# Kernel tuning notes

Measured on AMD Instinct MI355X. Metric: run time of the kernel, lower is better.

The kernel has to match this reference:

```python
import jax, jax.numpy as jnp
import numpy as np
from jax import lax

B, T, N, FI, FO, K = 32, 128, 200, 32, 64, 3
STRIDE, PAD, DIL = 1, 1, 1


def setup_inputs() -> dict:
    key = jax.random.key(0)
    k1, k2, k3 = jax.random.split(key, 3)
    bound = 1.0 / np.sqrt(FI * K)
    x = jax.random.normal(k1, (B, T, N, FI), dtype=jnp.float32)
    weight = jax.random.uniform(k2, (N * FO, FI, K), dtype=jnp.float32,
                                minval=-bound, maxval=bound)
    bias = jax.random.uniform(k3, (N, FO), dtype=jnp.float32,
                              minval=-bound, maxval=bound)
    return {"x": x, "weight": weight, "bias": bias}


def reference(x, weight, bias):
    # x: [B, T, N, FI] -> [B, N*FI, T]   (rearrange '... t n f -> ... (n f) t')
    b, t, n, fi = x.shape
    fo = bias.shape[1]
    xc = jnp.transpose(x, (0, 2, 3, 1)).reshape(b, n * fi, t)
    # Grouped conv1d: one group per instance (n groups), weight [N*FO, FI, K]
    out = lax.conv_general_dilated(
        xc, weight,
        window_strides=(STRIDE,),
        padding=[(PAD, PAD)],
        rhs_dilation=(DIL,),
        feature_group_count=n,
        dimension_numbers=("NCH", "OIH", "NCH"),
    )  # [B, N*FO, T_out]
    t_out = out.shape[-1]
    # rearrange '... (n f) t -> ... t n f'
    out = jnp.transpose(out.reshape(b, n, fo, t_out), (0, 3, 1, 2))
    return out + bias  # bias broadcasts over [B, T_out, N, FO]
```

## Files before the change

kernel.cpp:

```cpp
#include <hip/hip_runtime.h>
#include <hip/hip_bf16.h>
#include <cstddef>

#define B_ 32
#define T_ 128
#define N_ 200
#define FI_ 32
#define FO_ 64
#define K_ 3

typedef __attribute__((ext_vector_type(8))) short short8;
typedef __attribute__((ext_vector_type(8))) unsigned short ushort8;
typedef __attribute__((ext_vector_type(4))) float f32x4;

#define AROW_ 40
#define A_ROWS_ (T_ + 2)
#define B_OFF_ (A_ROWS_ * AROW_)
#define BROW_ 40
#define BK_SZ_ (FO_ * BROW_)

__device__ __forceinline__ unsigned short f2bf(float f) {
    union { __hip_bfloat16 h; unsigned short u; } cv;
    cv.h = __float2bfloat16(f);
    return cv.u;
}

__global__ void conv_prep(const float* __restrict__ w,
                          unsigned short* __restrict__ wbf) {
    const int idx = blockIdx.x * 256 + threadIdx.x;
    if (idx >= N_ * FO_) return;
    const float* wp = w + (size_t)idx * (FI_ * K_);
    float v[FI_ * K_];
    #pragma unroll
    for (int j = 0; j < (FI_ * K_) / 4; ++j) {
        const float4 t4 = *reinterpret_cast<const float4*>(&wp[j * 4]);
        v[j*4+0] = t4.x; v[j*4+1] = t4.y; v[j*4+2] = t4.z; v[j*4+3] = t4.w;
    }
    const int n = idx >> 6, f = idx & 63;
    #pragma unroll
    for (int tap = 0; tap < K_; ++tap) {
        ushort8 u[4];
        #pragma unroll
        for (int i = 0; i < FI_; ++i) u[i >> 3][i & 7] = f2bf(v[i * K_ + tap]);
        unsigned short* dst = wbf + (((size_t)n * K_ + tap) * FO_ + f) * FI_;
        #pragma unroll
        for (int q = 0; q < 4; ++q)
            *reinterpret_cast<ushort8*>(&dst[q * 8]) = u[q];
    }
}

template <bool PREW>
__global__ __launch_bounds__(256, 6) void conv_main(
    const float* __restrict__ x, const float* __restrict__ w,
    const unsigned short* __restrict__ wbf,
    const float* __restrict__ bias, float* __restrict__ out)
{
    __shared__ __align__(16) unsigned short lds[B_OFF_ + K_ * BK_SZ_];

    const int bid = blockIdx.x;
    const int b = bid & 31;
    const int n = bid >> 5;
    const int tid = threadIdx.x;
    const int lane = tid & 63;
    const int wv = tid >> 6;

    if constexpr (PREW) {
        const unsigned short* src = wbf + (size_t)n * K_ * FO_ * FI_;
        #pragma unroll
        for (int ss = 0; ss < 3; ++ss) {
            const int s = tid + ss * 256;
            const int tf = s >> 2;
            const int q = s & 3;
            const ushort8 u = *reinterpret_cast<const ushort8*>(&src[tf * FI_ + q * 8]);
            *reinterpret_cast<ushort8*>(
                &lds[B_OFF_ + (tf >> 6) * BK_SZ_ + (tf & 63) * BROW_ + q * 8]) = u;
        }
    } else {
        const int f = tid >> 2;
        const int i0 = (tid & 3) * 8;
        const float* wp = w + ((size_t)n * FO_ + f) * (FI_ * K_) + (size_t)i0 * K_;
        float v[24];
        #pragma unroll
        for (int j = 0; j < 6; ++j) {
            const float4 t4 = *reinterpret_cast<const float4*>(&wp[j * 4]);
            v[j*4+0] = t4.x; v[j*4+1] = t4.y; v[j*4+2] = t4.z; v[j*4+3] = t4.w;
        }
        #pragma unroll
        for (int k = 0; k < K_; ++k) {
            ushort8 u;
            #pragma unroll
            for (int j = 0; j < 8; ++j) u[j] = f2bf(v[j * K_ + k]);
            *reinterpret_cast<ushort8*>(&lds[B_OFF_ + k * BK_SZ_ + f * BROW_ + i0]) = u;
        }
    }

    const float* xb = x + ((size_t)b * T_ * N_ + n) * FI_;
    for (int s = tid; s < A_ROWS_ * 4; s += 256) {
        const int rr = s >> 2, q = s & 3;
        const int t = rr - 1;
        ushort8 u = (ushort8)0;
        if (t >= 0 && t < T_) {
            const float4 v0 = *reinterpret_cast<const float4*>(
                &xb[(size_t)t * N_ * FI_ + q * 8]);
            const float4 v1 = *reinterpret_cast<const float4*>(
                &xb[(size_t)t * N_ * FI_ + q * 8 + 4]);
            u[0] = f2bf(v0.x); u[1] = f2bf(v0.y); u[2] = f2bf(v0.z); u[3] = f2bf(v0.w);
            u[4] = f2bf(v1.x); u[5] = f2bf(v1.y); u[6] = f2bf(v1.z); u[7] = f2bf(v1.w);
        }
        *reinterpret_cast<ushort8*>(&lds[rr * AROW_ + q * 8]) = u;
    }

    __syncthreads();

    f32x4 acc[2][4];
    #pragma unroll
    for (int m = 0; m < 2; ++m)
        #pragma unroll
        for (int j = 0; j < 4; ++j)
            acc[m][j] = (f32x4){0.f, 0.f, 0.f, 0.f};

    const int row16 = lane & 15;
    const int grp = lane >> 4;

    #pragma unroll
    for (int k = 0; k < K_; ++k) {
        const short8 a0 = *reinterpret_cast<const short8*>(
            &lds[(wv * 32 + 0  + row16 + k) * AROW_ + grp * 8]);
        const short8 a1 = *reinterpret_cast<const short8*>(
            &lds[(wv * 32 + 16 + row16 + k) * AROW_ + grp * 8]);
        #pragma unroll
        for (int j = 0; j < 4; ++j) {
            const short8 bf = *reinterpret_cast<const short8*>(
                &lds[B_OFF_ + k * BK_SZ_ + (j * 16 + row16) * BROW_ + grp * 8]);
            acc[0][j] = __builtin_amdgcn_mfma_f32_16x16x32_bf16(a0, bf, acc[0][j], 0, 0, 0);
            acc[1][j] = __builtin_amdgcn_mfma_f32_16x16x32_bf16(a1, bf, acc[1][j], 0, 0, 0);
        }
    }

    #pragma unroll
    for (int j = 0; j < 4; ++j) {
        const float bv = bias[n * FO_ + j * 16 + row16];
        #pragma unroll
        for (int m = 0; m < 2; ++m) {
            #pragma unroll
            for (int r = 0; r < 4; ++r) {
                const int t = wv * 32 + m * 16 + grp * 4 + r;
                out[(((size_t)b * T_ + t) * N_ + n) * FO_ + j * 16 + row16] =
                    acc[m][j][r] + bv;
            }
        }
    }
}

extern "C" void kernel_launch(void* const* d_in, const int* in_sizes, int n_in,
                              void* d_out, int out_size, void* d_ws, size_t ws_size,
                              hipStream_t stream) {
    const float* x    = (const float*)d_in[0];
    const float* w    = (const float*)d_in[1];
    const float* bias = (const float*)d_in[2];
    float* out = (float*)d_out;

    const size_t W_BF_BYTES = (size_t)N_ * K_ * FO_ * FI_ * 2;
    const int grid = B_ * N_;

    if (ws_size >= W_BF_BYTES) {
        unsigned short* wbf = (unsigned short*)d_ws;
        conv_prep<<<(N_ * FO_ + 255) / 256, 256, 0, stream>>>(w, wbf);
        conv_main<true><<<grid, 256, 0, stream>>>(x, w, wbf, bias, out);
    } else {
        conv_main<false><<<grid, 256, 0, stream>>>(x, w, nullptr, bias, out);
    }
}
```

Baseline: 94.70 us.

## Load weight MFMA fragments directly from global memory instead of staging in LDS

The main kernel no longer copies the per-instance bf16 weight tile into shared memory. Each wave now reads its B-operand fragments straight from the prepacked global buffer, which L2 serves since all 32 batch blocks of an instance share the same weights. This shrinks LDS use from about 35 KB to about 10 KB per block, which could raise occupancy, and removes the LDS write/read round-trip. The prep kernel is also spread over four times more threads, each converting one 8-element chunk. The cost is redundant global and L2 traffic, since every wave reloads the weights, and MFMA issue may stall on global-memory latency.

```diff
diff --git a/kernel.cpp b/kernel.cpp
--- a/kernel.cpp
+++ b/kernel.cpp
@@ -15,9 +15,6 @@
 
 #define AROW_ 40
 #define A_ROWS_ (T_ + 2)
-#define B_OFF_ (A_ROWS_ * AROW_)
-#define BROW_ 40
-#define BK_SZ_ (FO_ * BROW_)
 
 __device__ __forceinline__ unsigned short f2bf(float f) {
     union { __hip_bfloat16 h; unsigned short u; } cv;
@@ -28,24 +25,25 @@
 __global__ void conv_prep(const float* __restrict__ w,
                           unsigned short* __restrict__ wbf) {
     const int idx = blockIdx.x * 256 + threadIdx.x;
-    if (idx >= N_ * FO_) return;
-    const float* wp = w + (size_t)idx * (FI_ * K_);
-    float v[FI_ * K_];
+    if (idx >= N_ * FO_ * 4) return;
+    const int q  = idx & 3;
+    const int nf = idx >> 2;
+    const int n = nf >> 6, f = nf & 63;
+
+    const float* wp = w + (size_t)nf * (FI_ * K_) + (size_t)q * 8 * K_;
+    float v[24];
     #pragma unroll
-    for (int j = 0; j < (FI_ * K_) / 4; ++j) {
+    for (int j = 0; j < 6; ++j) {
         const float4 t4 = *reinterpret_cast<const float4*>(&wp[j * 4]);
         v[j*4+0] = t4.x; v[j*4+1] = t4.y; v[j*4+2] = t4.z; v[j*4+3] = t4.w;
     }
-    const int n = idx >> 6, f = idx & 63;
     #pragma unroll
     for (int tap = 0; tap < K_; ++tap) {
-        ushort8 u[4];
+        ushort8 u;
         #pragma unroll
-        for (int i = 0; i < FI_; ++i) u[i >> 3][i & 7] = f2bf(v[i * K_ + tap]);
-        unsigned short* dst = wbf + (((size_t)n * K_ + tap) * FO_ + f) * FI_;
-        #pragma unroll
-        for (int q = 0; q < 4; ++q)
-            *reinterpret_cast<ushort8*>(&dst[q * 8]) = u[q];
+        for (int e = 0; e < 8; ++e) u[e] = f2bf(v[e * K_ + tap]);
+        *reinterpret_cast<ushort8*>(
+            &wbf[(((size_t)n * K_ + tap) * FO_ + f) * FI_ + q * 8]) = u;
     }
 }
 
@@ -55,7 +53,7 @@
     const unsigned short* __restrict__ wbf,
     const float* __restrict__ bias, float* __restrict__ out)
 {
-    __shared__ __align__(16) unsigned short lds[B_OFF_ + K_ * BK_SZ_];
+    __shared__ __align__(16) unsigned short lds[A_ROWS_ * AROW_];
 
     const int bid = blockIdx.x;
     const int b = bid & 31;
@@ -63,36 +61,8 @@
     const int tid = threadIdx.x;
     const int lane = tid & 63;
     const int wv = tid >> 6;
-
-    if constexpr (PREW) {
-        const unsigned short* src = wbf + (size_t)n * K_ * FO_ * FI_;
-        #pragma unroll
-        for (int ss = 0; ss < 3; ++ss) {
-            const int s = tid + ss * 256;
-            const int tf = s >> 2;
-            const int q = s & 3;
-            const ushort8 u = *reinterpret_cast<const ushort8*>(&src[tf * FI_ + q * 8]);
-            *reinterpret_cast<ushort8*>(
-                &lds[B_OFF_ + (tf >> 6) * BK_SZ_ + (tf & 63) * BROW_ + q * 8]) = u;
-        }
-    } else {
-        const int f = tid >> 2;
-        const int i0 = (tid & 3) * 8;
-        const float* wp = w + ((size_t)n * FO_ + f) * (FI_ * K_) + (size_t)i0 * K_;
-        float v[24];
-        #pragma unroll
-        for (int j = 0; j < 6; ++j) {
-            const float4 t4 = *reinterpret_cast<const float4*>(&wp[j * 4]);
-            v[j*4+0] = t4.x; v[j*4+1] = t4.y; v[j*4+2] = t4.z; v[j*4+3] = t4.w;
-        }
-        #pragma unroll
-        for (int k = 0; k < K_; ++k) {
-            ushort8 u;
-            #pragma unroll
-            for (int j = 0; j < 8; ++j) u[j] = f2bf(v[j * K_ + k]);
-            *reinterpret_cast<ushort8*>(&lds[B_OFF_ + k * BK_SZ_ + f * BROW_ + i0]) = u;
-        }
-    }
+    const int row16 = lane & 15;
+    const int grp = lane >> 4;
 
     const float* xb = x + ((size_t)b * T_ * N_ + n) * FI_;
     for (int s = tid; s < A_ROWS_ * 4; s += 256) {
@@ -119,21 +89,34 @@
         for (int j = 0; j < 4; ++j)
             acc[m][j] = (f32x4){0.f, 0.f, 0.f, 0.f};
 
-    const int row16 = lane & 15;
-    const int grp = lane >> 4;
-
     #pragma unroll
     for (int k = 0; k < K_; ++k) {
         const short8 a0 = *reinterpret_cast<const short8*>(
             &lds[(wv * 32 + 0  + row16 + k) * AROW_ + grp * 8]);
         const short8 a1 = *reinterpret_cast<const short8*>(
             &lds[(wv * 32 + 16 + row16 + k) * AROW_ + grp * 8]);
+        short8 bfr[4];
+        if constexpr (PREW) {
+            #pragma unroll
+            for (int j = 0; j < 4; ++j)
+                bfr[j] = *reinterpret_cast<const short8*>(
+                    &wbf[(((size_t)n * K_ + k) * FO_ + j * 16 + row16) * FI_ + grp * 8]);
+        } else {
+            #pragma unroll
+            for (int j = 0; j < 4; ++j) {
+                const float* wp = &w[((size_t)(n * FO_ + j * 16 + row16)) * (FI_ * K_)
+                                     + grp * 8 * K_];
+                ushort8 u;
+                #pragma unroll
+                for (int e = 0; e < 8; ++e) u[e] = f2bf(wp[e * K_ + k]);
+                union { ushort8 u8; short8 s8; } cv; cv.u8 = u;
+                bfr[j] = cv.s8;
+            }
+        }
         #pragma unroll
         for (int j = 0; j < 4; ++j) {
-            const short8 bf = *reinterpret_cast<const short8*>(
-                &lds[B_OFF_ + k * BK_SZ_ + (j * 16 + row16) * BROW_ + grp * 8]);
-            acc[0][j] = __builtin_amdgcn_mfma_f32_16x16x32_bf16(a0, bf, acc[0][j], 0, 0, 0);
-            acc[1][j] = __builtin_amdgcn_mfma_f32_16x16x32_bf16(a1, bf, acc[1][j], 0, 0, 0);
+            acc[0][j] = __builtin_amdgcn_mfma_f32_16x16x32_bf16(a0, bfr[j], acc[0][j], 0, 0, 0);
+            acc[1][j] = __builtin_amdgcn_mfma_f32_16x16x32_bf16(a1, bfr[j], acc[1][j], 0, 0, 0);
         }
     }
 
@@ -165,7 +148,7 @@
 
     if (ws_size >= W_BF_BYTES) {
         unsigned short* wbf = (unsigned short*)d_ws;
-        conv_prep<<<(N_ * FO_ + 255) / 256, 256, 0, stream>>>(w, wbf);
+        conv_prep<<<(N_ * FO_ * 4 + 255) / 256, 256, 0, stream>>>(w, wbf);
         conv_main<true><<<grid, 256, 0, stream>>>(x, w, wbf, bias, out);
     } else {
         conv_main<false><<<grid, 256, 0, stream>>>(x, w, nullptr, bias, out);
```

After: 98.77 us. 4.3% more time.
